# Kernel tuning notes

Measured on AMD Instinct MI355X. Metric: run time of the kernel, lower is better.

## Reference

```python
import jax, jax.numpy as jnp
import numpy as np
from jax import lax

KSIZE = 7

def _grid():
    # torch.linspace(-7//2, 7//2, 7) == linspace(-4, 3, 7): asymmetric, step 7/6
    x = np.linspace(-4.0, 3.0, KSIZE, dtype=np.float32).reshape(-1, 1)
    y = x.T
    return x, y

def _gaussian_kernel(sigma):
    x, y = _grid()
    g = np.exp(-(x ** 2 + y ** 2) / (2.0 * sigma ** 2))
    g = g / g.sum()
    return g.reshape(1, 1, KSIZE, KSIZE).astype(np.float32)

def _log_kernel(sigma):
    x, y = _grid()
    r2 = x ** 2 + y ** 2
    log = (1.0 - r2 / (2.0 * sigma ** 2)) * np.exp(-r2 / (2.0 * sigma ** 2))
    log = log / np.abs(log).sum()
    return log.reshape(1, 1, KSIZE, KSIZE).astype(np.float32)

SOBEL_X = jnp.asarray([[-1, 0, 1], [-2, 0, 2], [-1, 0, 1]], dtype=jnp.float32).reshape(1, 1, 3, 3)
SOBEL_Y = jnp.asarray([[-1, -2, -1], [0, 0, 0], [1, 2, 1]], dtype=jnp.float32).reshape(1, 1, 3, 3)
POINT = jnp.asarray([[0, -1, 0], [-1, 4, -1], [0, -1, 0]], dtype=jnp.float32).reshape(1, 1, 3, 3)
STRUCT_FILTERS = [jnp.asarray(_gaussian_kernel(s)) for s in (0.5, 1.0, 2.0)]
SCALE_FILTERS = [jnp.asarray(_log_kernel(s)) for s in (1.0, 2.0, 4.0)]

def _conv(x, k, pad):
    # torch F.conv2d == cross-correlation, which lax conv also computes (no kernel flip)
    return lax.conv_general_dilated(
        x, k, window_strides=(1, 1),
        padding=[(pad, pad), (pad, pad)],
        dimension_numbers=("NCHW", "OIHW", "NCHW"))

def _mse(a, b):
    d = a - b
    return jnp.mean(d * d)

def _maxpool3(x):
    # torch max_pool2d pads with -inf
    return lax.reduce_window(
        x, -jnp.inf, lax.max,
        window_dimensions=(1, 1, 3, 3), window_strides=(1, 1, 1, 1),
        padding=[(0, 0), (0, 0), (1, 1), (1, 1)])

def setup_inputs() -> dict:
    key = jax.random.key(0)
    k1, k2 = jax.random.split(key)
    shape = (64, 1, 512, 512)
    return {
        "reconstruction": jax.random.normal(k1, shape, dtype=jnp.float32),
        "target": jax.random.normal(k2, shape, dtype=jnp.float32),
    }

def reference(reconstruction, target):
    # intensity-weighted reconstruction loss
    w = (target > target.mean()).astype(reconstruction.dtype) * 2.0 + 1.0
    recon_loss = _mse(reconstruction * w, target * w)

    # gradient (sobel) loss
    gradient_loss = (
        _mse(_conv(reconstruction, SOBEL_X, 1), _conv(target, SOBEL_X, 1)) +
        _mse(_conv(reconstruction, SOBEL_Y, 1), _conv(target, SOBEL_Y, 1)))

    # point-source (laplacian) loss
    point_loss = _mse(_conv(reconstruction, POINT, 1), _conv(target, POINT, 1))

    # multi-scale gaussian structure loss
    structure_loss = 0.0
    for f in STRUCT_FILTERS:
        structure_loss += _mse(_conv(reconstruction, f, KSIZE // 2), _conv(target, f, KSIZE // 2))

    # LoG blob-scale loss
    scale_loss = 0.0
    for f in SCALE_FILTERS:
        scale_loss += _mse(_conv(reconstruction, f, KSIZE // 2), _conv(target, f, KSIZE // 2))

    # peak preservation via 3x3 max pool + L1
    peak_loss = jnp.mean(jnp.abs(_maxpool3(reconstruction) - _maxpool3(target)))

    return (recon_loss + 2.0 * gradient_loss + 1.5 * point_loss +
            1.0 * structure_loss + 1.0 * scale_loss + 2.0 * peak_loss)
```

## Files before the change

### kernel.cpp

```cpp
#include <hip/hip_runtime.h>
#include <math.h>

#define IMG 512
#define IMG2 (IMG * IMG)
#define NPIX (64 * IMG2)
#define ZPB 8

__device__ float g_c[64];

typedef __fp16 h2_t __attribute__((ext_vector_type(2)));

__device__ __forceinline__ float rdfl(float x) {
    return __uint_as_float(__builtin_amdgcn_readfirstlane(__float_as_uint(x)));
}
__device__ __forceinline__ unsigned int rdflu(float x) {
    return __builtin_amdgcn_readfirstlane(__float_as_uint(x));
}
__device__ __forceinline__ unsigned int as_u(h2_t h) {
    union { h2_t h; unsigned int u; } c;
    c.h = h;
    return c.u;
}
__device__ __forceinline__ h2_t as_h2(unsigned int u) {
    union { unsigned int u; h2_t h; } c;
    c.u = u;
    return c.h;
}
__device__ __forceinline__ h2_t h2z() {
    h2_t z = {(__fp16)0.f, (__fp16)0.f};
    return z;
}
__device__ __forceinline__ h2_t hmax2(h2_t a, h2_t b) {
    return __builtin_elementwise_max(a, b);
}

__device__ void compute_coeffs() {
    const double step = 7.0 / 6.0;
    float x[7];
    for (int j = 0; j < 7; j++) x[j] = (float)(-4.0 + j * step);
    x[6] = 3.0f;
    const float sigs[4] = {0.5f, 1.0f, 2.0f, 4.0f};
    float E[4][7], Q[4][7], Vv[3][7];
    for (int s = 0; s < 4; s++) {
        float inv = 1.0f / (2.0f * sigs[s] * sigs[s]);
        for (int j = 0; j < 7; j++) {
            float q = x[j] * x[j] * inv;
            Q[s][j] = q;
            E[s][j] = expf(-q);
        }
    }
    for (int s = 0; s < 3; s++)
        for (int j = 0; j < 7; j++) Vv[s][j] = Q[s + 1][j] * E[s + 1][j];

    auto pk2 = [](float a, float b) -> float {
        h2_t h;
        h[0] = (__fp16)a;
        h[1] = (__fp16)b;
        union { h2_t h; float f; } c;
        c.h = h;
        return c.f;
    };
    for (int k = 0; k < 7; k++) {
        g_c[k] = pk2(E[0][k], E[1][k]);
        g_c[7 + k] = pk2(E[2][k], E[3][k]);
        g_c[14 + k] = pk2(Vv[0][k], Vv[1][k]);
        g_c[21 + k] = pk2(Vv[2][k], Vv[2][k]);
        g_c[28 + k] = pk2(E[1][k], E[2][k]);
        g_c[35 + k] = pk2(E[2][k], -Vv[2][k]);
        g_c[42 + k] = pk2(-Vv[0][k], -Vv[1][k]);
        g_c[49 + k] = pk2(E[3][k], 0.f);
    }
    for (int s = 0; s < 3; s++) {
        float gs = 0.f;
        for (int i = 0; i < 7; i++)
            for (int j = 0; j < 7; j++) gs += E[s][i] * E[s][j];
        g_c[56 + s] = 1.0f / (gs * gs);
    }
    for (int s = 1; s < 4; s++) {
        float n = 0.f;
        for (int i = 0; i < 7; i++)
            for (int j = 0; j < 7; j++) {
                float v = E[s][i] * E[s][j] * (1.0f - Q[s][i] - Q[s][j]);
                n += fabsf(v);
            }
        g_c[59 + (s - 1)] = 1.0f / (n * n);
    }
}

__global__ __launch_bounds__(256) void sum_target_kernel(const float4* __restrict__ t4,
                                                          float* __restrict__ ws) {
    if (blockIdx.x == 0 && threadIdx.x == 0) compute_coeffs();
    float s = 0.f;
    for (int i = blockIdx.x * 256 + threadIdx.x; i < NPIX / 4; i += 256 * 256) {
        float4 v = t4[i];
        s += (v.x + v.y) + (v.z + v.w);
    }
    for (int off = 32; off > 0; off >>= 1) s += __shfl_down(s, off);
    __shared__ float ps[4];
    int lane = threadIdx.x & 63, wid = threadIdx.x >> 6;
    if (lane == 0) ps[wid] = s;
    __syncthreads();
    if (threadIdx.x == 0) ws[blockIdx.x] = (ps[0] + ps[1]) + (ps[2] + ps[3]);
}

__global__ __launch_bounds__(256, 5) void main_kernel(const float* __restrict__ R,
                                                      const float* __restrict__ T,
                                                      float* __restrict__ ws) {
    __shared__ float sd[38][44];
    __shared__ unsigned srt[34][44];
    __shared__ uint4 hrec[32][39];
    __shared__ float red[4];

    const int tid = threadIdx.x;
    const int gx0 = blockIdx.x * 32, gy0 = blockIdx.y * 32;
    const int z0 = blockIdx.z * ZPB;
    const int bid = blockIdx.x + (blockIdx.y << 4) + (blockIdx.z << 8);

    {
        float v = ws[tid];
        for (int off = 32; off > 0; off >>= 1) v += __shfl_down(v, off);
        int lane = tid & 63, wid = tid >> 6;
        if (lane == 0) red[wid] = v;
        __syncthreads();
    }
    const float mean = rdfl(((red[0] + red[1]) + (red[2] + red[3])) * (1.0f / (float)NPIX));

    h2_t cE01[7], cE23[7], cV01[7], cV2[7], d2c[7], d3c[7], d4c[7], d5c[7];
#pragma unroll
    for (int k = 0; k < 7; k++) {
        cE01[k] = as_h2(rdflu(g_c[k]));
        cE23[k] = as_h2(rdflu(g_c[7 + k]));
        cV01[k] = as_h2(rdflu(g_c[14 + k]));
        cV2[k] = as_h2(rdflu(g_c[21 + k]));
        d2c[k] = as_h2(rdflu(g_c[28 + k]));
        d3c[k] = as_h2(rdflu(g_c[35 + k]));
        d4c[k] = as_h2(rdflu(g_c[42 + k]));
        d5c[k] = as_h2(rdflu(g_c[49 + k]));
    }
    float invS4[3], invN2[3];
#pragma unroll
    for (int s = 0; s < 3; s++) {
        invS4[s] = rdfl(g_c[56 + s]);
        invN2[s] = rdfl(g_c[59 + s]);
    }

    const int q0 = tid, q1 = tid + 256;
    const bool has1 = (q1 < 380);
    const int i0 = q0 / 10, c0 = q0 - 10 * i0;
    const int i1 = q1 / 10, c1 = q1 - 10 * i1;
    const int gy_0 = gy0 + i0 - 3, gxb0 = gx0 - 4 + 4 * c0;
    const int gy_1 = gy0 + i1 - 3, gxb1 = gx0 - 4 + 4 * c1;
    const int o0 = min(max(gy_0, 0), IMG - 1) * IMG + min(max(gxb0, 0), IMG - 4);
    const int o1 = min(max(gy_1, 0), IMG - 1) * IMG + min(max(gxb1, 0), IMG - 4);
    const bool vy0 = ((unsigned)gy_0 < IMG), vy1 = ((unsigned)gy_1 < IMG);
    bool m0[4], m1[4];
#pragma unroll
    for (int e = 0; e < 4; e++) {
        m0[e] = vy0 && ((unsigned)(gxb0 + e) < IMG);
        m1[e] = vy1 && ((unsigned)(gxb1 + e) < IMG);
    }

    const int x = tid & 31;
    const int y0 = (tid >> 5) * 4;

    float4 ra, ta, rb, tb;

#define LOAD_TILE(zz)                          \
    {                                          \
        const float* Rz = R + (long)(zz)*IMG2; \
        const float* Tz = T + (long)(zz)*IMG2; \
        ra = *(const float4*)(Rz + o0);        \
        ta = *(const float4*)(Tz + o0);        \
        if (has1) {                            \
            rb = *(const float4*)(Rz + o1);    \
            tb = *(const float4*)(Tz + o1);    \
        }                                      \
    }

#define WRITE_TILE()                                                                 \
    {                                                                                \
        float rv[4] = {ra.x, ra.y, ra.z, ra.w};                                      \
        float tv[4] = {ta.x, ta.y, ta.z, ta.w};                                      \
        float dq[4];                                                                 \
        unsigned pkq[4];                                                             \
        _Pragma("unroll") for (int e = 0; e < 4; e++) {                              \
            dq[e] = m0[e] ? (rv[e] - tv[e]) : 0.f;                                   \
            h2_t h = __builtin_amdgcn_cvt_pkrtz(rv[e], tv[e]);                       \
            pkq[e] = m0[e] ? as_u(h) : 0xFC00FC00u;                                  \
        }                                                                            \
        *(float4*)&sd[i0][4 * c0] = make_float4(dq[0], dq[1], dq[2], dq[3]);         \
        if (i0 >= 2 && i0 < 36)                                                      \
            *(uint4*)&srt[i0 - 2][4 * c0] = make_uint4(pkq[0], pkq[1], pkq[2], pkq[3]); \
        if (has1) {                                                                  \
            float rv1[4] = {rb.x, rb.y, rb.z, rb.w};                                 \
            float tv1[4] = {tb.x, tb.y, tb.z, tb.w};                                 \
            float dq1[4];                                                            \
            unsigned pkq1[4];                                                        \
            _Pragma("unroll") for (int e = 0; e < 4; e++) {                          \
                dq1[e] = m1[e] ? (rv1[e] - tv1[e]) : 0.f;                            \
                h2_t h = __builtin_amdgcn_cvt_pkrtz(rv1[e], tv1[e]);                 \
                pkq1[e] = m1[e] ? as_u(h) : 0xFC00FC00u;                             \
            }                                                                        \
            *(float4*)&sd[i1][4 * c1] = make_float4(dq1[0], dq1[1], dq1[2], dq1[3]); \
            if (i1 >= 2 && i1 < 36)                                                  \
                *(uint4*)&srt[i1 - 2][4 * c1] =                                      \
                    make_uint4(pkq1[0], pkq1[1], pkq1[2], pkq1[3]);                  \
        }                                                                            \
    }

    LOAD_TILE(z0);
    WRITE_TILE();
    __syncthreads();

    float total = 0.f;

    for (int it = 0; it < ZPB; ++it) {
        const bool havenext = (it + 1 < ZPB);
        if (havenext) LOAD_TILE(z0 + it + 1);

        {
            float dw[6][3];
#pragma unroll
            for (int r = 0; r < 6; r++)
#pragma unroll
                for (int c = 0; c < 3; c++) dw[r][c] = sd[y0 + 2 + r][x + 3 + c];
            float rx[6], rs[6];
#pragma unroll
            for (int r = 0; r < 6; r++) {
                rx[r] = dw[r][2] - dw[r][0];
                rs[r] = dw[r][0] + 2.f * dw[r][1] + dw[r][2];
            }
            h2_t cm[6];
            float tc[6];
#pragma unroll
            for (int r = 0; r < 6; r++) {
                h2_t a = as_h2(srt[y0 + r][x + 3]);
                h2_t b = as_h2(srt[y0 + r][x + 4]);
                h2_t c = as_h2(srt[y0 + r][x + 5]);
                cm[r] = hmax2(hmax2(a, b), c);
                tc[r] = (float)b[1];
            }
#pragma unroll
            for (int yy = 0; yy < 4; yy++) {
                float sx = rx[yy] + 2.f * rx[yy + 1] + rx[yy + 2];
                float sy = rs[yy + 2] - rs[yy];
                float pt = 4.f * dw[yy + 1][1] - dw[yy][1] - dw[yy + 2][1] - dw[yy + 1][0] -
                           dw[yy + 1][2];
                float d = dw[yy + 1][1];
                float w2 = (tc[yy + 1] > mean) ? 9.f : 1.f;
                h2_t wm = hmax2(hmax2(cm[yy], cm[yy + 1]), cm[yy + 2]);
                float mr = (float)wm[0], mt = (float)wm[1];
                total += w2 * d * d + 2.f * (sx * sx + sy * sy) + 1.5f * pt * pt +
                         2.f * fabsf(mr - mt);
            }
        }

        for (int j = tid; j < 304; j += 256) {
            int xq = j / 38, y = j - 38 * xq;
            const float* rp = &sd[y][4 * xq];
            float4 A = *(const float4*)(rp);
            float4 B = *(const float4*)(rp + 4);
            float4 C = *(const float4*)(rp + 8);
            float w[12] = {A.x, A.y, A.z, A.w, B.x, B.y, B.z, B.w, C.x, C.y, C.z, C.w};
            h2_t wp[12];
#pragma unroll
            for (int i = 0; i < 12; i++) wp[i] = __builtin_amdgcn_cvt_pkrtz(w[i], w[i]);
#pragma unroll
            for (int p = 0; p < 4; p++) {
                h2_t aE01 = h2z(), aE23 = h2z(), aV01 = h2z(), aV2 = h2z();
#pragma unroll
                for (int k = 0; k < 7; k++) {
                    h2_t d = wp[p + 1 + k];
                    aE01 = cE01[k] * d + aE01;
                    aE23 = cE23[k] * d + aE23;
                    aV01 = cV01[k] * d + aV01;
                    aV2 = cV2[k] * d + aV2;
                }
                h2_t he12 = __builtin_shufflevector(aE01, aE23, 1, 2);
                h2_t tm01 = he12 - aV01;
                h2_t he33 = __builtin_shufflevector(aE23, aE23, 1, 1);
                h2_t tm22 = he33 - aV2;
                hrec[4 * xq + p][y] =
                    make_uint4(as_u(aE01), as_u(aE23), as_u(tm01), as_u(tm22));
            }
        }
        __syncthreads();

        if (havenext) WRITE_TILE();

        {
            h2_t A1[4], A2[4], A3[4], A4[4], A5[4];
#pragma unroll
            for (int yy = 0; yy < 4; yy++) {
                A1[yy] = h2z();
                A2[yy] = h2z();
                A3[yy] = h2z();
                A4[yy] = h2z();
                A5[yy] = h2z();
            }
#pragma unroll
            for (int q = 0; q < 10; q++) {
                uint4 rec = hrec[x][y0 + q];
                h2_t rx = as_h2(rec.x), ry = as_h2(rec.y);
                h2_t rz = as_h2(rec.z), rw = as_h2(rec.w);
                h2_t r12 = __builtin_shufflevector(rx, ry, 1, 2);
#pragma unroll
                for (int yy = 0; yy < 4; yy++) {
                    const int k = q - yy;
                    if (k >= 0 && k <= 6) {
                        A1[yy] = cE01[k] * rx + A1[yy];
                        A2[yy] = d2c[k] * rz + A2[yy];
                        A3[yy] = d3c[k] * ry + A3[yy];
                        A4[yy] = d4c[k] * r12 + A4[yy];
                        A5[yy] = d5c[k] * rw + A5[yy];
                    }
                }
            }
#pragma unroll
            for (int yy = 0; yy < 4; yy++) {
                h2_t Bp = A2[yy] + A4[yy];
                float g0 = (float)A1[yy][0], g1 = (float)A1[yy][1];
                float g2 = (float)A3[yy][0];
                float aL0 = (float)Bp[0], aL1 = (float)Bp[1];
                float aL2 = (float)A5[yy][0] + (float)A3[yy][1];
                total += invS4[0] * g0 * g0 + invS4[1] * g1 * g1 + invS4[2] * g2 * g2 +
                         invN2[0] * aL0 * aL0 + invN2[1] * aL1 * aL1 + invN2[2] * aL2 * aL2;
            }
        }
        __syncthreads();
    }

    for (int off = 32; off > 0; off >>= 1) total += __shfl_down(total, off);
    int lane = tid & 63, wid = tid >> 6;
    if (lane == 0) red[wid] = total;
    __syncthreads();
    if (tid == 0) ws[256 + bid] = (red[0] + red[1]) + (red[2] + red[3]);
}

__global__ __launch_bounds__(256) void finalize_kernel(const float* __restrict__ ws,
                                                       float* __restrict__ out) {
    float s = 0.f;
    for (int i = threadIdx.x; i < 2048; i += 256) s += ws[256 + i];
    for (int off = 32; off > 0; off >>= 1) s += __shfl_down(s, off);
    __shared__ float ps[4];
    int lane = threadIdx.x & 63, wid = threadIdx.x >> 6;
    if (lane == 0) ps[wid] = s;
    __syncthreads();
    if (threadIdx.x == 0)
        out[0] = ((ps[0] + ps[1]) + (ps[2] + ps[3])) * (1.0f / (float)NPIX);
}

extern "C" void kernel_launch(void* const* d_in, const int* in_sizes, int n_in,
                              void* d_out, int out_size, void* d_ws, size_t ws_size,
                              hipStream_t stream) {
    const float* recon = (const float*)d_in[0];
    const float* target = (const float*)d_in[1];
    float* ws = (float*)d_ws;

    hipLaunchKernelGGL(sum_target_kernel, dim3(256), dim3(256), 0, stream,
                       (const float4*)target, ws);
    dim3 grid(16, 16, 64 / ZPB), block(256);
    hipLaunchKernelGGL(main_kernel, grid, block, 0, stream, recon, target, ws);
    hipLaunchKernelGGL(finalize_kernel, dim3(1), dim3(256), 0, stream, ws, (float*)d_out);
}
```

Measured before the change: 108.1 us.

## Drop fp32 difference tile, derive differences from packed fp16 tile

Removes the fp32 shared-memory difference array and stores only the packed fp16 (recon,target) tile, extended to the full halo. The Sobel, Laplacian and MSE differences, and the inputs to the 7x7 separable pass, are now computed in fp16 from the packed pairs. Launch bounds rise to 6 blocks per SM because the shared footprint is smaller. This reduces LDS usage and writes and raises occupancy, but lowers precision: the differences are now formed after rounding each input to fp16 and the 3x3 stencils accumulate in fp16. The out-of-bounds pad value changes from -inf to the most negative finite half so padded differences come out as zero.

After: 110.2 us. About the same (+1.9%).

```diff
diff --git a/kernel.cpp b/kernel.cpp
--- a/kernel.cpp
+++ b/kernel.cpp
@@ -9,6 +9,8 @@
 __device__ float g_c[64];
 
 typedef __fp16 h2_t __attribute__((ext_vector_type(2)));
+
+#define OOB_SRT 0xFBFFFBFFu
 
 __device__ __forceinline__ float rdfl(float x) {
     return __uint_as_float(__builtin_amdgcn_readfirstlane(__float_as_uint(x)));
@@ -103,11 +105,10 @@
     if (threadIdx.x == 0) ws[blockIdx.x] = (ps[0] + ps[1]) + (ps[2] + ps[3]);
 }
 
-__global__ __launch_bounds__(256, 5) void main_kernel(const float* __restrict__ R,
+__global__ __launch_bounds__(256, 6) void main_kernel(const float* __restrict__ R,
                                                       const float* __restrict__ T,
                                                       float* __restrict__ ws) {
-    __shared__ float sd[38][44];
-    __shared__ unsigned srt[34][44];
+    __shared__ unsigned srt[38][44];
     __shared__ uint4 hrec[32][39];
     __shared__ float red[4];
 
@@ -177,35 +178,24 @@
         }                                      \
     }
 
-#define WRITE_TILE()                                                                 \
-    {                                                                                \
-        float rv[4] = {ra.x, ra.y, ra.z, ra.w};                                      \
-        float tv[4] = {ta.x, ta.y, ta.z, ta.w};                                      \
-        float dq[4];                                                                 \
-        unsigned pkq[4];                                                             \
-        _Pragma("unroll") for (int e = 0; e < 4; e++) {                              \
-            dq[e] = m0[e] ? (rv[e] - tv[e]) : 0.f;                                   \
-            h2_t h = __builtin_amdgcn_cvt_pkrtz(rv[e], tv[e]);                       \
-            pkq[e] = m0[e] ? as_u(h) : 0xFC00FC00u;                                  \
-        }                                                                            \
-        *(float4*)&sd[i0][4 * c0] = make_float4(dq[0], dq[1], dq[2], dq[3]);         \
-        if (i0 >= 2 && i0 < 36)                                                      \
-            *(uint4*)&srt[i0 - 2][4 * c0] = make_uint4(pkq[0], pkq[1], pkq[2], pkq[3]); \
-        if (has1) {                                                                  \
-            float rv1[4] = {rb.x, rb.y, rb.z, rb.w};                                 \
-            float tv1[4] = {tb.x, tb.y, tb.z, tb.w};                                 \
-            float dq1[4];                                                            \
-            unsigned pkq1[4];                                                        \
-            _Pragma("unroll") for (int e = 0; e < 4; e++) {                          \
-                dq1[e] = m1[e] ? (rv1[e] - tv1[e]) : 0.f;                            \
-                h2_t h = __builtin_amdgcn_cvt_pkrtz(rv1[e], tv1[e]);                 \
-                pkq1[e] = m1[e] ? as_u(h) : 0xFC00FC00u;                             \
-            }                                                                        \
-            *(float4*)&sd[i1][4 * c1] = make_float4(dq1[0], dq1[1], dq1[2], dq1[3]); \
-            if (i1 >= 2 && i1 < 36)                                                  \
-                *(uint4*)&srt[i1 - 2][4 * c1] =                                      \
-                    make_uint4(pkq1[0], pkq1[1], pkq1[2], pkq1[3]);                  \
-        }                                                                            \
+#define WRITE_TILE()                                                            \
+    {                                                                           \
+        unsigned pkq[4];                                                        \
+        _Pragma("unroll") for (int e = 0; e < 4; e++) {                         \
+            float rv = ((const float*)&ra)[e], tv = ((const float*)&ta)[e];     \
+            pkq[e] = m0[e] ? as_u(__builtin_amdgcn_cvt_pkrtz(rv, tv)) : OOB_SRT; \
+        }                                                                       \
+        *(uint4*)&srt[i0][4 * c0] = make_uint4(pkq[0], pkq[1], pkq[2], pkq[3]); \
+        if (has1) {                                                             \
+            unsigned pkq1[4];                                                   \
+            _Pragma("unroll") for (int e = 0; e < 4; e++) {                     \
+                float rv = ((const float*)&rb)[e], tv = ((const float*)&tb)[e]; \
+                pkq1[e] =                                                       \
+                    m1[e] ? as_u(__builtin_amdgcn_cvt_pkrtz(rv, tv)) : OOB_SRT; \
+            }                                                                   \
+            *(uint4*)&srt[i1][4 * c1] =                                         \
+                make_uint4(pkq1[0], pkq1[1], pkq1[2], pkq1[3]);                 \
+        }                                                                       \
     }
 
     LOAD_TILE(z0);
@@ -219,34 +209,34 @@
         if (havenext) LOAD_TILE(z0 + it + 1);
 
         {
-            float dw[6][3];
+            h2_t w_[6][3];
 #pragma unroll
             for (int r = 0; r < 6; r++)
 #pragma unroll
-                for (int c = 0; c < 3; c++) dw[r][c] = sd[y0 + 2 + r][x + 3 + c];
-            float rx[6], rs[6];
-#pragma unroll
-            for (int r = 0; r < 6; r++) {
-                rx[r] = dw[r][2] - dw[r][0];
-                rs[r] = dw[r][0] + 2.f * dw[r][1] + dw[r][2];
-            }
+                for (int c = 0; c < 3; c++) w_[r][c] = as_h2(srt[y0 + 2 + r][x + 3 + c]);
+            __fp16 dcol[6][3];
             h2_t cm[6];
             float tc[6];
 #pragma unroll
             for (int r = 0; r < 6; r++) {
-                h2_t a = as_h2(srt[y0 + r][x + 3]);
-                h2_t b = as_h2(srt[y0 + r][x + 4]);
-                h2_t c = as_h2(srt[y0 + r][x + 5]);
-                cm[r] = hmax2(hmax2(a, b), c);
-                tc[r] = (float)b[1];
+#pragma unroll
+                for (int c = 0; c < 3; c++) dcol[r][c] = w_[r][c][0] - w_[r][c][1];
+                cm[r] = hmax2(hmax2(w_[r][0], w_[r][1]), w_[r][2]);
+                tc[r] = (float)w_[r][1][1];
+            }
+            __fp16 rx[6], rs[6];
+#pragma unroll
+            for (int r = 0; r < 6; r++) {
+                rx[r] = dcol[r][2] - dcol[r][0];
+                rs[r] = dcol[r][0] + (__fp16)2.f * dcol[r][1] + dcol[r][2];
             }
 #pragma unroll
             for (int yy = 0; yy < 4; yy++) {
-                float sx = rx[yy] + 2.f * rx[yy + 1] + rx[yy + 2];
-                float sy = rs[yy + 2] - rs[yy];
-                float pt = 4.f * dw[yy + 1][1] - dw[yy][1] - dw[yy + 2][1] - dw[yy + 1][0] -
-                           dw[yy + 1][2];
-                float d = dw[yy + 1][1];
+                float sx = (float)(rx[yy] + (__fp16)2.f * rx[yy + 1] + rx[yy + 2]);
+                float sy = (float)(rs[yy + 2] - rs[yy]);
+                float pt = (float)((__fp16)4.f * dcol[yy + 1][1] - dcol[yy][1] -
+                                   dcol[yy + 2][1] - dcol[yy + 1][0] - dcol[yy + 1][2]);
+                float d = (float)dcol[yy + 1][1];
                 float w2 = (tc[yy + 1] > mean) ? 9.f : 1.f;
                 h2_t wm = hmax2(hmax2(cm[yy], cm[yy + 1]), cm[yy + 2]);
                 float mr = (float)wm[0], mt = (float)wm[1];
@@ -257,20 +247,27 @@
 
         for (int j = tid; j < 304; j += 256) {
             int xq = j / 38, y = j - 38 * xq;
-            const float* rp = &sd[y][4 * xq];
-            float4 A = *(const float4*)(rp);
-            float4 B = *(const float4*)(rp + 4);
-            float4 C = *(const float4*)(rp + 8);
-            float w[12] = {A.x, A.y, A.z, A.w, B.x, B.y, B.z, B.w, C.x, C.y, C.z, C.w};
-            h2_t wp[12];
-#pragma unroll
-            for (int i = 0; i < 12; i++) wp[i] = __builtin_amdgcn_cvt_pkrtz(w[i], w[i]);
+            const unsigned* rp = &srt[y][4 * xq];
+            uint4 A = *(const uint4*)(rp);
+            uint4 B = *(const uint4*)(rp + 4);
+            uint4 C = *(const uint4*)(rp + 8);
+            unsigned uw[12] = {A.x, A.y, A.z, A.w, B.x, B.y, B.z, B.w, C.x, C.y, C.z, C.w};
+            h2_t wp[10];
+#pragma unroll
+            for (int i = 0; i < 10; i++) {
+                h2_t v = as_h2(uw[i + 1]);
+                __fp16 d = v[0] - v[1];
+                h2_t dd;
+                dd[0] = d;
+                dd[1] = d;
+                wp[i] = dd;
+            }
 #pragma unroll
             for (int p = 0; p < 4; p++) {
                 h2_t aE01 = h2z(), aE23 = h2z(), aV01 = h2z(), aV2 = h2z();
 #pragma unroll
                 for (int k = 0; k < 7; k++) {
-                    h2_t d = wp[p + 1 + k];
+                    h2_t d = wp[p + k];
                     aE01 = cE01[k] * d + aE01;
                     aE23 = cE23[k] * d + aE23;
                     aV01 = cV01[k] * d + aV01;
```
